# Performance work log

Hardware: AMD Instinct MI355X
Metric: run time of the kernel (lower is better)

## Reference

```python
import jax, jax.numpy as jnp
import numpy as np

D_MODEL, N_HEAD, D_HEAD = 1024, 16, 64
QLEN, MLEN, BSZ = 1024, 512, 4
KLEN = QLEN + MLEN
RLEN = QLEN + KLEN
SCALE = 1.0 / (D_HEAD ** 0.5)
LN_EPS = 1e-12


def rel_shift(x, klen):
    # x: [i, j, b, n] -> shifted [i, klen, b, n]
    i, j, b, n = x.shape
    x = x.reshape(j, i, b, n)[1:].reshape(i, j - 1, b, n)
    return x[:, :klen]


def layer_norm(x, gamma, beta, eps=LN_EPS):
    mu = jnp.mean(x, axis=-1, keepdims=True)
    var = jnp.mean(jnp.square(x - mu), axis=-1, keepdims=True)
    return (x - mu) * jax.lax.rsqrt(var + eps) * gamma + beta


def setup_inputs() -> dict:
    key = jax.random.key(0)
    ks = jax.random.split(key, 16)
    std = 0.02
    h = jax.random.normal(ks[0], (QLEN, BSZ, D_MODEL), jnp.float32)
    r = jax.random.normal(ks[1], (RLEN, BSZ, D_MODEL), jnp.float32)
    mems = jax.random.normal(ks[2], (MLEN, BSZ, D_MODEL), jnp.float32)
    # binary float mask (1 = masked), broadcast over head dim
    attn_mask = (jax.random.uniform(ks[3], (QLEN, KLEN, BSZ, 1)) < 0.1).astype(jnp.float32)
    # one-hot segment matrix over 2 segment classes
    seg_ids = jax.random.randint(ks[4], (QLEN, KLEN, BSZ), 0, 2)
    seg_mat = jax.nn.one_hot(seg_ids, 2, dtype=jnp.float32)
    Wq = std * jax.random.normal(ks[5], (D_MODEL, N_HEAD, D_HEAD), jnp.float32)
    Wk = std * jax.random.normal(ks[6], (D_MODEL, N_HEAD, D_HEAD), jnp.float32)
    Wv = std * jax.random.normal(ks[7], (D_MODEL, N_HEAD, D_HEAD), jnp.float32)
    Wo = std * jax.random.normal(ks[8], (D_MODEL, N_HEAD, D_HEAD), jnp.float32)
    Wr = std * jax.random.normal(ks[9], (D_MODEL, N_HEAD, D_HEAD), jnp.float32)
    r_w_bias = jnp.zeros((N_HEAD, D_HEAD), jnp.float32)
    r_r_bias = jnp.zeros((N_HEAD, D_HEAD), jnp.float32)
    r_s_bias = jnp.zeros((N_HEAD, D_HEAD), jnp.float32)
    seg_embed = std * jax.random.normal(ks[10], (2, N_HEAD, D_HEAD), jnp.float32)
    ln_gamma = jnp.ones((D_MODEL,), jnp.float32)
    ln_beta = jnp.zeros((D_MODEL,), jnp.float32)
    return dict(h=h, r=r, mems=mems, attn_mask=attn_mask, seg_mat=seg_mat,
                Wq=Wq, Wk=Wk, Wv=Wv, Wo=Wo, Wr=Wr,
                r_w_bias=r_w_bias, r_r_bias=r_r_bias, r_s_bias=r_s_bias,
                seg_embed=seg_embed, ln_gamma=ln_gamma, ln_beta=ln_beta)


def reference(h, r, mems, attn_mask, seg_mat, Wq, Wk, Wv, Wo, Wr,
              r_w_bias, r_r_bias, r_s_bias, seg_embed, ln_gamma, ln_beta):
    cat = jnp.concatenate([mems, h], axis=0)  # [klen, b, d_model]
    q_head = jnp.einsum('ibh,hnd->ibnd', h, Wq)
    k_head_h = jnp.einsum('jbh,hnd->jbnd', cat, Wk)
    v_head_h = jnp.einsum('jbh,hnd->jbnd', cat, Wv)
    k_head_r = jnp.einsum('jbh,hnd->jbnd', r, Wr)

    klen = k_head_h.shape[0]
    ac = jnp.einsum('ibnd,jbnd->ijbn', q_head + r_w_bias, k_head_h)
    bd = jnp.einsum('ibnd,jbnd->ijbn', q_head + r_r_bias, k_head_r)
    bd = rel_shift(bd, klen)
    ef = jnp.einsum('ibnd,snd->ibns', q_head + r_s_bias, seg_embed)
    ef = jnp.einsum('ijbs,ibns->ijbn', seg_mat, ef)

    attn_score = (ac + bd + ef) * SCALE - 1e30 * attn_mask
    attn_prob = jax.nn.softmax(attn_score, axis=1)
    attn_vec = jnp.einsum('ijbn,jbnd->ibnd', attn_prob, v_head_h)

    attn_out = jnp.einsum('ibnd,hnd->ibh', attn_vec, Wo) + h  # residual
    return layer_norm(attn_out, ln_gamma, ln_beta)
```

## Files before the change

### kernel.cpp

```cpp
#include <hip/hip_runtime.h>

typedef unsigned short u16;
typedef __attribute__((ext_vector_type(8))) short bf16x8;
typedef __attribute__((ext_vector_type(4))) float f32x4;

constexpr int DM = 1024;
constexpr int NH = 16;
constexpr int DH = 64;
constexpr int QL = 1024;
constexpr int ML = 512;
constexpr int KL = 1536;
constexpr int RL = 2560;
constexpr int BS = 4;
constexpr int JT = KL / 64;
constexpr float SCALE = 0.125f;

static __device__ __forceinline__ u16 f2bf(float f) {
    unsigned u = __float_as_uint(f);
    u += 0x7fffu + ((u >> 16) & 1u);
    return (u16)(u >> 16);
}

static __device__ __forceinline__ void glds16(const u16* g, u16* l) {
    __builtin_amdgcn_global_load_lds(
        (const __attribute__((address_space(1))) unsigned int*)g,
        (__attribute__((address_space(3))) unsigned int*)l,
        16, 0, 0);
}

__global__ __launch_bounds__(256) void prep_kernel(
    const float* __restrict__ mems, const float* __restrict__ h,
    const float* __restrict__ r, const float* __restrict__ Wo,
    const float* __restrict__ mask, const float* __restrict__ segm,
    const float* __restrict__ Wq, const float* __restrict__ Wk,
    const float* __restrict__ Wv, const float* __restrict__ Wr,
    u16* __restrict__ catb, u16* __restrict__ rb, u16* __restrict__ wob,
    u16* __restrict__ WqT, u16* __restrict__ WkT,
    u16* __restrict__ WvT, u16* __restrict__ WrT,
    ulonglong2* __restrict__ pk)
{
    __shared__ float smem[64 * 65];
    const int id = blockIdx.x;
    const int t = threadIdx.x;

    if (id < 17408) {
        const long C0 = (long)ML * BS * DM;
        const long C1 = (long)KL * BS * DM;
        const long C2 = C1 + (long)RL * BS * DM;
        long g = ((long)id * 256 + t) * 4;
        const float* src; u16* dst;
        if (g < C0)      { src = mems + g;        dst = catb + g; }
        else if (g < C1) { src = h + (g - C0);    dst = catb + g; }
        else if (g < C2) { src = r + (g - C1);    dst = rb + (g - C1); }
        else             { src = Wo + (g - C2);   dst = wob + (g - C2); }
        float4 v = *(const float4*)src;
        unsigned lo = (unsigned)f2bf(v.x) | ((unsigned)f2bf(v.y) << 16);
        unsigned hi = (unsigned)f2bf(v.z) | ((unsigned)f2bf(v.w) << 16);
        *(uint2*)dst = make_uint2(lo, hi);
        return;
    }
    if (id < 18432) {
        float (*tile)[65] = (float(*)[65])smem;
        const int local = id - 17408;
        const float* W; u16* WT;
        switch (local >> 8) {
            case 0:  W = Wq; WT = WqT; break;
            case 1:  W = Wk; WT = WkT; break;
            case 2:  W = Wv; WT = WvT; break;
            default: W = Wr; WT = WrT; break;
        }
        const int k0 = (local & 15) * 64, n0 = ((local >> 4) & 15) * 64;
        const int tr = t >> 6, tc = t & 63;
        #pragma unroll
        for (int rr = 0; rr < 16; rr++) {
            int rw = tr + rr * 4;
            tile[rw][tc] = W[(size_t)(k0 + rw) * DM + n0 + tc];
        }
        __syncthreads();
        #pragma unroll
        for (int rr = 0; rr < 16; rr++) {
            int n = tr + rr * 4;
            WT[(size_t)(n0 + n) * DM + k0 + tc] = f2bf(tile[tc][n]);
        }
        return;
    }
    {
        float* mk = smem;
        float* sg = smem + 256;
        const int local = id - 18432;
        const int i = local / JT, jt = local - i * JT;
        const size_t base = ((size_t)i * KL + jt * 64) * BS;
        mk[t] = mask[base + t];
        float2 s2 = ((const float2*)(segm + base * 2))[t];
        sg[t] = s2.y;
        __syncthreads();
        const int b = t >> 6, lane = t & 63;
        const unsigned long long mb = __ballot(mk[lane * 4 + b] > 0.5f);
        const unsigned long long sb = __ballot(sg[lane * 4 + b] > 0.5f);
        if (lane == 0) {
            ulonglong2 v; v.x = mb; v.y = sb;
            pk[((size_t)b * QL + i) * JT + jt] = v;
        }
    }
}

__global__ __launch_bounds__(256) void proj_kernel(
    const u16* __restrict__ hb, const u16* __restrict__ catb,
    const u16* __restrict__ rb,
    const u16* __restrict__ WqT, const u16* __restrict__ WkT,
    const u16* __restrict__ WvT, const u16* __restrict__ WrT,
    float* __restrict__ q_s, u16* __restrict__ k_s,
    u16* __restrict__ v_s, u16* __restrict__ kr_s)
{
    __shared__ u16 a_lds[128][32];
    __shared__ u16 b_lds[128][32];
    const int id = blockIdx.x;
    const u16 *A, *B; void* C; int SEQ, MODE, local;
    if (id < 256)       { A = hb;   B = WqT; C = q_s;  SEQ = QL; MODE = 1; local = id; }
    else if (id < 640)  { A = catb; B = WkT; C = k_s;  SEQ = KL; MODE = 2; local = id - 256; }
    else if (id < 1024) { A = catb; B = WvT; C = v_s;  SEQ = KL; MODE = 2; local = id - 640; }
    else                { A = rb;   B = WrT; C = kr_s; SEQ = RL; MODE = 2; local = id - 1024; }
    const int bm = local >> 3, bnn = local & 7;

    const int t = threadIdx.x;
    const int w = t >> 6, lane = t & 63, l15 = lane & 15, q4 = lane >> 4;
    const int wm = (w >> 1) * 64, wn = (w & 1) * 64;
    const int srow = w * 32 + (lane >> 2);
    const int scol = (lane & 3) * 8;
    const u16* Ab = A + (size_t)(bm * 128 + srow) * DM + scol;
    const u16* Bb = B + (size_t)(bnn * 128 + srow) * DM + scol;
    u16* a_dst = &a_lds[w * 32][0];
    u16* b_dst = &b_lds[w * 32][0];

    f32x4 acc[4][4] = {};

    for (int k0 = 0; k0 < DM; k0 += 32) {
        __syncthreads();
        glds16(Ab + k0,           a_dst);
        glds16(Ab + k0 + 16 * DM, a_dst + 16 * 32);
        glds16(Bb + k0,           b_dst);
        glds16(Bb + k0 + 16 * DM, b_dst + 16 * 32);
        __syncthreads();
        bf16x8 af[4], bf[4];
        #pragma unroll
        for (int rt = 0; rt < 4; rt++)
            af[rt] = *(const bf16x8*)&a_lds[wm + rt * 16 + l15][q4 * 8];
        #pragma unroll
        for (int ct = 0; ct < 4; ct++)
            bf[ct] = *(const bf16x8*)&b_lds[wn + ct * 16 + l15][q4 * 8];
        #pragma unroll
        for (int rt = 0; rt < 4; rt++)
            #pragma unroll
            for (int ct = 0; ct < 4; ct++)
                acc[rt][ct] = __builtin_amdgcn_mfma_f32_16x16x32_bf16(
                    af[rt], bf[ct], acc[rt][ct], 0, 0, 0);
    }

    #pragma unroll
    for (int rt = 0; rt < 4; rt++)
      #pragma unroll
      for (int ct = 0; ct < 4; ct++)
        #pragma unroll
        for (int rg = 0; rg < 4; rg++) {
            const int R = bm * 128 + wm + rt * 16 + q4 * 4 + rg;
            const int Cc = bnn * 128 + wn + ct * 16 + l15;
            const float v = acc[rt][ct][rg];
            const int sq = R >> 2, bb = R & 3, hn = Cc >> 6, dd = Cc & 63;
            const size_t idx = ((size_t)(bb * NH + hn) * SEQ + sq) * DH + dd;
            if (MODE == 1) ((float*)C)[idx] = v;
            else           ((u16*)C)[idx]  = f2bf(v);
        }
}

__global__ __launch_bounds__(256) void vtrans_kernel(
    const u16* __restrict__ v_s, u16* __restrict__ vt_s)
{
    __shared__ u16 tl[64][72];
    const int j0 = blockIdx.x * 64;
    const int bn = blockIdx.y;
    const u16* vin = v_s + (size_t)bn * KL * DH;
    u16* vout = vt_s + (size_t)bn * DH * KL;
    const int t = threadIdx.x;
    const int r = t >> 3, c8 = (t & 7) * 8;
    #pragma unroll
    for (int it = 0; it < 64; it += 32)
        *(uint4*)&tl[r + it][c8] = *(const uint4*)(vin + (size_t)(j0 + r + it) * DH + c8);
    __syncthreads();
    #pragma unroll
    for (int it = 0; it < 64; it += 32) {
        const int d = r + it;
        u16 tmp[8];
        #pragma unroll
        for (int jj = 0; jj < 8; jj++) tmp[jj] = tl[c8 + jj][d];
        *(uint4*)&vout[(size_t)d * KL + j0 + c8] = *(const uint4*)tmp;
    }
}

__global__ __launch_bounds__(256) void ogemm_kernel(
    const u16* __restrict__ A, const u16* __restrict__ B,
    float* __restrict__ Cout)
{
    __shared__ u16 a_lds[128][32];
    __shared__ u16 b_lds[128][32];
    const int bm = blockIdx.x, bnn = blockIdx.y;
    const int t = threadIdx.x;
    const int w = t >> 6, lane = t & 63, l15 = lane & 15, q4 = lane >> 4;
    const int wm = (w >> 1) * 64, wn = (w & 1) * 64;
    const int srow = w * 32 + (lane >> 2);
    const int scol = (lane & 3) * 8;
    const u16* Ab = A + (size_t)(bm * 128 + srow) * DM + scol;
    const u16* Bb = B + (size_t)(bnn * 128 + srow) * DM + scol;
    u16* a_dst = &a_lds[w * 32][0];
    u16* b_dst = &b_lds[w * 32][0];

    f32x4 acc[4][4] = {};

    for (int k0 = 0; k0 < DM; k0 += 32) {
        __syncthreads();
        glds16(Ab + k0,           a_dst);
        glds16(Ab + k0 + 16 * DM, a_dst + 16 * 32);
        glds16(Bb + k0,           b_dst);
        glds16(Bb + k0 + 16 * DM, b_dst + 16 * 32);
        __syncthreads();
        bf16x8 af[4], bf[4];
        #pragma unroll
        for (int rt = 0; rt < 4; rt++)
            af[rt] = *(const bf16x8*)&a_lds[wm + rt * 16 + l15][q4 * 8];
        #pragma unroll
        for (int ct = 0; ct < 4; ct++)
            bf[ct] = *(const bf16x8*)&b_lds[wn + ct * 16 + l15][q4 * 8];
        #pragma unroll
        for (int rt = 0; rt < 4; rt++)
            #pragma unroll
            for (int ct = 0; ct < 4; ct++)
                acc[rt][ct] = __builtin_amdgcn_mfma_f32_16x16x32_bf16(
                    af[rt], bf[ct], acc[rt][ct], 0, 0, 0);
    }

    #pragma unroll
    for (int rt = 0; rt < 4; rt++)
      #pragma unroll
      for (int ct = 0; ct < 4; ct++)
        #pragma unroll
        for (int rg = 0; rg < 4; rg++) {
            const int R = bm * 128 + wm + rt * 16 + q4 * 4 + rg;
            const int C = bnn * 128 + wn + ct * 16 + l15;
            Cout[(size_t)R * DM + C] = acc[rt][ct][rg];
        }
}

__global__ __launch_bounds__(256, 3) void attn_kernel(
    const float* __restrict__ q_s, const u16* __restrict__ k_s,
    const u16* __restrict__ vt_s, const u16* __restrict__ kr_s,
    const ulonglong2* __restrict__ pk,
    const float* __restrict__ rwb, const float* __restrict__ rrb,
    const float* __restrict__ rsb, const float* __restrict__ seg_embed,
    u16* __restrict__ av_s)
{
    __shared__ u16 k2[2][64][32];
    __shared__ u16 vt2[2][64][32];
    __shared__ u16 krl[128][64];
    __shared__ u16 p_lds[4][16][72];
    __shared__ float e_lds[2][64];

    const int bn = blockIdx.x;
    const int itile = blockIdx.y;
    const int b = bn >> 4, n = bn & 15;
    const int t = threadIdx.x;
    const int w = t >> 6, lane = t & 63, l15 = lane & 15, q4 = lane >> 4;
    const int i0 = itile * 64;
    const int ib = i0 + w * 16;

    const float* q_bn = q_s + (size_t)bn * QL * DH;
    const u16* k_bn   = k_s  + (size_t)bn * KL * DH;
    const u16* vt_bn  = vt_s + (size_t)bn * DH * KL;
    const u16* kr_bn  = kr_s + (size_t)bn * RL * DH;
    const ulonglong2* pk_b = pk + (size_t)b * QL * JT;

    if (t < 128) {
        const int rr = t >> 1, s = t & 1;
        const float* qrow = q_bn + (size_t)(i0 + rr) * DH;
        const float* se = seg_embed + (s * NH + n) * DH;
        const float* bias = rsb + n * DH;
        float acc = 0.f;
        #pragma unroll 16
        for (int d = 0; d < DH; d++) acc += (qrow[d] + bias[d]) * se[d];
        e_lds[s][rr] = acc;
    }

    bf16x8 qw[2], qr[2];
    {
        const float* qrow = q_bn + (size_t)(ib + l15) * DH;
        const float* bw = rwb + n * DH;
        const float* br = rrb + n * DH;
        #pragma unroll
        for (int kk = 0; kk < 2; kk++) {
            const int dbase = kk * 32 + q4 * 8;
            #pragma unroll
            for (int j = 0; j < 8; j++) {
                float qv = qrow[dbase + j];
                qw[kk][j] = (short)f2bf(qv + bw[dbase + j]);
                qr[kk][j] = (short)f2bf(qv + br[dbase + j]);
            }
        }
    }

    const int srow = lane >> 2;
    const int sseg = (lane & 3) * 8;
    const u16* kg = k_bn  + (size_t)(w * 16 + srow) * DH + sseg;
    const u16* vg = vt_bn + (size_t)(w * 16 + srow) * KL + sseg;
    u16* kd0 = &k2[0][w * 16][0];
    u16* kd1 = &k2[1][w * 16][0];
    u16* vd0 = &vt2[0][w * 16][0];
    u16* vd1 = &vt2[1][w * 16][0];

    const int krow = lane >> 3;
    const int ksrcseg = (lane & 7) ^ krow;
    u16* krd = &krl[w * 32][0];

    f32x4 o[4] = {};
    float l_r[4] = {0.f, 0.f, 0.f, 0.f};

    const int lrb = 48 - w * 16 + l15;
    const int sA = ((q4)     ^ (l15 & 7)) * 8;
    const int sB = ((q4 + 4) ^ (l15 & 7)) * 8;

    for (int jt = 0; jt < JT; jt++) {
        const int j0 = jt * 64;
        const int Pbase = j0 + QL - i0 - 63;
        __syncthreads();
        glds16(kg + (size_t)j0 * DH,      kd0);
        glds16(kg + (size_t)j0 * DH + 32, kd1);
        glds16(vg + j0,                   vd0);
        glds16(vg + j0 + 32,              vd1);
        {
            const u16* krg = kr_bn + (size_t)(Pbase + w * 32 + krow) * DH + ksrcseg * 8;
            #pragma unroll
            for (int m = 0; m < 4; m++)
                glds16(krg + (size_t)m * 8 * DH, krd + m * 8 * 64);
        }
        ulonglong2 mp[4];
        #pragma unroll
        for (int rg = 0; rg < 4; rg++)
            mp[rg] = pk_b[(size_t)(ib + q4 * 4 + rg) * JT + jt];
        __syncthreads();

        f32x4 sac[4] = {};
        #pragma unroll
        for (int ct = 0; ct < 4; ct++) {
            bf16x8 kb0 = *(const bf16x8*)&k2[0][ct * 16 + l15][q4 * 8];
            bf16x8 kb1 = *(const bf16x8*)&k2[1][ct * 16 + l15][q4 * 8];
            sac[ct] = __builtin_amdgcn_mfma_f32_16x16x32_bf16(qw[0], kb0, sac[ct], 0, 0, 0);
            sac[ct] = __builtin_amdgcn_mfma_f32_16x16x32_bf16(qw[1], kb1, sac[ct], 0, 0, 0);
        }

        f32x4 bacc[5] = {};
        #pragma unroll
        for (int wc = 0; wc < 5; wc++) {
            bf16x8 b0 = *(const bf16x8*)&krl[lrb + wc * 16][sA];
            bf16x8 b1 = *(const bf16x8*)&krl[lrb + wc * 16][sB];
            bacc[wc] = __builtin_amdgcn_mfma_f32_16x16x32_bf16(qr[0], b0, bacc[wc], 0, 0, 0);
            bacc[wc] = __builtin_amdgcn_mfma_f32_16x16x32_bf16(qr[1], b1, bacc[wc], 0, 0, 0);
        }

        #pragma unroll
        for (int rg = 0; rg < 4; rg++) {
            const int row = q4 * 4 + rg;
            const int v = l15 + 15 - row;
            const int srcl = (q4 << 4) | (v & 15);
            float sh[5];
            #pragma unroll
            for (int w5 = 0; w5 < 5; w5++)
                sh[w5] = __shfl(bacc[w5][rg], srcl, 64);
            const float e0 = e_lds[0][w * 16 + row];
            const float e1 = e_lds[1][w * 16 + row];
            float s0 = 0.f;
            #pragma unroll
            for (int ct = 0; ct < 4; ct++) {
                const float bd = (v < 16) ? sh[ct] : sh[ct + 1];
                const int bit = ct * 16 + l15;
                const float ef = ((mp[rg].y >> bit) & 1ull) ? e1 : e0;
                const float s = (sac[ct][rg] + bd + ef) * SCALE;
                float p = __expf(s);
                p = ((mp[rg].x >> bit) & 1ull) ? 0.f : p;
                p_lds[w][row][ct * 16 + l15] = f2bf(p);
                s0 += p;
            }
            l_r[rg] += s0;
        }

        #pragma unroll
        for (int kk = 0; kk < 2; kk++) {
            bf16x8 pf = *(const bf16x8*)&p_lds[w][l15][kk * 32 + q4 * 8];
            #pragma unroll
            for (int dt = 0; dt < 4; dt++) {
                bf16x8 vf = *(const bf16x8*)&vt2[kk][dt * 16 + l15][q4 * 8];
                o[dt] = __builtin_amdgcn_mfma_f32_16x16x32_bf16(pf, vf, o[dt], 0, 0, 0);
            }
        }
    }

    #pragma unroll
    for (int rg = 0; rg < 4; rg++) {
        #pragma unroll
        for (int off = 1; off < 16; off <<= 1)
            l_r[rg] += __shfl_xor(l_r[rg], off, 64);
        l_r[rg] = 1.f / l_r[rg];
    }
    #pragma unroll
    for (int dt = 0; dt < 4; dt++)
        #pragma unroll
        for (int rg = 0; rg < 4; rg++) {
            const int row = q4 * 4 + rg;
            const int ii = ib + row;
            const int d = dt * 16 + l15;
            const float v = o[dt][rg] * l_r[rg];
            av_s[(size_t)(ii * BS + b) * DM + n * DH + d] = f2bf(v);
        }
}

__global__ __launch_bounds__(256) void ln_kernel(
    const float* __restrict__ ao, const float* __restrict__ h,
    const float* __restrict__ gamma, const float* __restrict__ beta,
    float* __restrict__ out)
{
    __shared__ float red[8];
    const int row = blockIdx.x, t = threadIdx.x;
    const float* a  = ao + (size_t)row * DM;
    const float* hh = h  + (size_t)row * DM;
    float4 av = *(const float4*)(a + t * 4);
    float4 hv = *(const float4*)(hh + t * 4);
    const float x0 = av.x + hv.x, x1 = av.y + hv.y;
    const float x2 = av.z + hv.z, x3 = av.w + hv.w;
    float s = x0 + x1 + x2 + x3;
    float s2 = x0 * x0 + x1 * x1 + x2 * x2 + x3 * x3;
    #pragma unroll
    for (int off = 1; off < 64; off <<= 1) {
        s  += __shfl_xor(s, off, 64);
        s2 += __shfl_xor(s2, off, 64);
    }
    const int w = t >> 6;
    if ((t & 63) == 0) { red[w] = s; red[4 + w] = s2; }
    __syncthreads();
    s  = red[0] + red[1] + red[2] + red[3];
    s2 = red[4] + red[5] + red[6] + red[7];
    const float mu = s * (1.f / DM);
    const float var = s2 * (1.f / DM) - mu * mu;
    const float rstd = rsqrtf(var + 1e-12f);
    float4 g  = *(const float4*)(gamma + t * 4);
    float4 bb = *(const float4*)(beta + t * 4);
    float4 ov;
    ov.x = (x0 - mu) * rstd * g.x + bb.x;
    ov.y = (x1 - mu) * rstd * g.y + bb.y;
    ov.z = (x2 - mu) * rstd * g.z + bb.z;
    ov.w = (x3 - mu) * rstd * g.w + bb.w;
    *(float4*)(out + (size_t)row * DM + t * 4) = ov;
}

extern "C" void kernel_launch(void* const* d_in, const int* in_sizes, int n_in,
                              void* d_out, int out_size, void* d_ws, size_t ws_size,
                              hipStream_t stream) {
    (void)in_sizes; (void)n_in; (void)out_size; (void)ws_size;
    const float* h    = (const float*)d_in[0];
    const float* r    = (const float*)d_in[1];
    const float* mems = (const float*)d_in[2];
    const float* mask = (const float*)d_in[3];
    const float* segm = (const float*)d_in[4];
    const float* Wq   = (const float*)d_in[5];
    const float* Wk   = (const float*)d_in[6];
    const float* Wv   = (const float*)d_in[7];
    const float* Wo   = (const float*)d_in[8];
    const float* Wr   = (const float*)d_in[9];
    const float* rwb  = (const float*)d_in[10];
    const float* rrb  = (const float*)d_in[11];
    const float* rsb  = (const float*)d_in[12];
    const float* semb = (const float*)d_in[13];
    const float* gam  = (const float*)d_in[14];
    const float* bet  = (const float*)d_in[15];
    float* out = (float*)d_out;

    char* wsb = (char*)d_ws;
    size_t off = 0;
    auto alloc = [&](size_t bytes) -> void* {
        void* p = wsb + off; off += (bytes + 255) & ~(size_t)255; return p;
    };
    u16* catb = (u16*)alloc((size_t)KL * BS * DM * 2);
    u16* rb   = (u16*)alloc((size_t)RL * BS * DM * 2);
    u16* WqT  = (u16*)alloc((size_t)DM * DM * 2);
    u16* WkT  = (u16*)alloc((size_t)DM * DM * 2);
    u16* WvT  = (u16*)alloc((size_t)DM * DM * 2);
    u16* WrT  = (u16*)alloc((size_t)DM * DM * 2);
    u16* WoB  = (u16*)alloc((size_t)DM * DM * 2);
    float* q_s = (float*)alloc((size_t)BS * NH * QL * DH * 4);
    u16* k_s  = (u16*)alloc((size_t)BS * NH * KL * DH * 2);
    u16* vt_s = (u16*)alloc((size_t)BS * NH * KL * DH * 2);
    u16* kr_s = (u16*)alloc((size_t)BS * NH * RL * DH * 2 + 8192);
    u16* av_s = (u16*)alloc((size_t)QL * BS * DM * 2);
    float* ao_s = (float*)alloc((size_t)QL * BS * DM * 4);
    ulonglong2* pk = (ulonglong2*)alloc((size_t)BS * QL * JT * 16);
    u16* v_s = (u16*)ao_s;

    prep_kernel<<<43008, 256, 0, stream>>>(mems, h, r, Wo, mask, segm,
                                           Wq, Wk, Wv, Wr,
                                           catb, rb, WoB,
                                           WqT, WkT, WvT, WrT, pk);
    const u16* hb = catb + (size_t)2048 * DM;
    proj_kernel<<<1664, 256, 0, stream>>>(hb, catb, rb, WqT, WkT, WvT, WrT,
                                          q_s, k_s, v_s, kr_s);
    vtrans_kernel<<<dim3(JT, 64), 256, 0, stream>>>(v_s, vt_s);
    attn_kernel<<<dim3(64, 16), 256, 0, stream>>>(q_s, k_s, vt_s, kr_s, pk,
                                                  rwb, rrb, rsb, semb, av_s);
    ogemm_kernel<<<dim3(32, 8), 256, 0, stream>>>(av_s, WoB, ao_s);
    ln_kernel<<<4096, 256, 0, stream>>>(ao_s, h, gam, bet, out);
}
```

Baseline: 530.0 us.

## Enlarge attention query tile to 128 rows with 8 warps sharing K/V loads

```diff
diff --git a/kernel.cpp b/kernel.cpp
--- a/kernel.cpp
+++ b/kernel.cpp
@@ -249,7 +249,7 @@
         }
 }
 
-__global__ __launch_bounds__(256, 3) void attn_kernel(
+__global__ __launch_bounds__(512, 4) void attn_kernel(
     const float* __restrict__ q_s, const u16* __restrict__ k_s,
     const u16* __restrict__ vt_s, const u16* __restrict__ kr_s,
     const ulonglong2* __restrict__ pk,
@@ -259,16 +259,15 @@
 {
     __shared__ u16 k2[2][64][32];
     __shared__ u16 vt2[2][64][32];
-    __shared__ u16 krl[128][64];
-    __shared__ u16 p_lds[4][16][72];
-    __shared__ float e_lds[2][64];
+    __shared__ u16 krl[256][64];
+    __shared__ u16 p_lds[8][16][72];
+    __shared__ float e_lds[2][128];
 
     const int bn = blockIdx.x;
-    const int itile = blockIdx.y;
     const int b = bn >> 4, n = bn & 15;
     const int t = threadIdx.x;
     const int w = t >> 6, lane = t & 63, l15 = lane & 15, q4 = lane >> 4;
-    const int i0 = itile * 64;
+    const int i0 = blockIdx.y * 128;
     const int ib = i0 + w * 16;
 
     const float* q_bn = q_s + (size_t)bn * QL * DH;
@@ -277,7 +276,7 @@
     const u16* kr_bn  = kr_s + (size_t)bn * RL * DH;
     const ulonglong2* pk_b = pk + (size_t)b * QL * JT;
 
-    if (t < 128) {
+    if (t < 256) {
         const int rr = t >> 1, s = t & 1;
         const float* qrow = q_bn + (size_t)(i0 + rr) * DH;
         const float* se = seg_embed + (s * NH + n) * DH;
@@ -307,37 +306,39 @@
 
     const int srow = lane >> 2;
     const int sseg = (lane & 3) * 8;
-    const u16* kg = k_bn  + (size_t)(w * 16 + srow) * DH + sseg;
-    const u16* vg = vt_bn + (size_t)(w * 16 + srow) * KL + sseg;
-    u16* kd0 = &k2[0][w * 16][0];
-    u16* kd1 = &k2[1][w * 16][0];
-    u16* vd0 = &vt2[0][w * 16][0];
-    u16* vd1 = &vt2[1][w * 16][0];
-
     const int krow = lane >> 3;
     const int ksrcseg = (lane & 7) ^ krow;
-    u16* krd = &krl[w * 32][0];
 
     f32x4 o[4] = {};
     float l_r[4] = {0.f, 0.f, 0.f, 0.f};
 
-    const int lrb = 48 - w * 16 + l15;
+    const int lrb = 144 - w * 16 + l15;
     const int sA = ((q4)     ^ (l15 & 7)) * 8;
     const int sB = ((q4 + 4) ^ (l15 & 7)) * 8;
 
     for (int jt = 0; jt < JT; jt++) {
         const int j0 = jt * 64;
-        const int Pbase = j0 + QL - i0 - 63;
-        __syncthreads();
-        glds16(kg + (size_t)j0 * DH,      kd0);
-        glds16(kg + (size_t)j0 * DH + 32, kd1);
-        glds16(vg + j0,                   vd0);
-        glds16(vg + j0 + 32,              vd1);
-        {
-            const u16* krg = kr_bn + (size_t)(Pbase + w * 32 + krow) * DH + ksrcseg * 8;
-            #pragma unroll
-            for (int m = 0; m < 4; m++)
-                glds16(krg + (size_t)m * 8 * DH, krd + m * 8 * 64);
+        const int Pbase = j0 + QL - i0 - 159;
+        __syncthreads();
+        if (w < 4) {
+            #pragma unroll
+            for (int g = 0; g < 4; g++) {
+                const int rr = g * 16 + srow;
+                if (w == 0)
+                    glds16(k_bn + (size_t)(j0 + rr) * DH + sseg,       &k2[0][g * 16][0]);
+                else if (w == 1)
+                    glds16(k_bn + (size_t)(j0 + rr) * DH + 32 + sseg,  &k2[1][g * 16][0]);
+                else if (w == 2)
+                    glds16(vt_bn + (size_t)rr * KL + j0 + sseg,        &vt2[0][g * 16][0]);
+                else
+                    glds16(vt_bn + (size_t)rr * KL + j0 + 32 + sseg,   &vt2[1][g * 16][0]);
+            }
+        } else {
+            const int rbase = (w - 4) * 64;
+            const u16* krg = kr_bn + ((size_t)(Pbase + rbase + krow)) * DH + ksrcseg * 8;
+            #pragma unroll
+            for (int g = 0; g < 8; g++)
+                glds16(krg + (size_t)g * 8 * DH, &krl[rbase + g * 8][0]);
         }
         ulonglong2 mp[4];
         #pragma unroll
@@ -494,7 +495,8 @@
     float* q_s = (float*)alloc((size_t)BS * NH * QL * DH * 4);
     u16* k_s  = (u16*)alloc((size_t)BS * NH * KL * DH * 2);
     u16* vt_s = (u16*)alloc((size_t)BS * NH * KL * DH * 2);
-    u16* kr_s = (u16*)alloc((size_t)BS * NH * RL * DH * 2 + 8192);
+    (void)alloc(32768);
+    u16* kr_s = (u16*)alloc((size_t)BS * NH * RL * DH * 2 + 16384);
     u16* av_s = (u16*)alloc((size_t)QL * BS * DM * 2);
     float* ao_s = (float*)alloc((size_t)QL * BS * DM * 4);
     ulonglong2* pk = (ulonglong2*)alloc((size_t)BS * QL * JT * 16);
@@ -508,8 +510,8 @@
     proj_kernel<<<1664, 256, 0, stream>>>(hb, catb, rb, WqT, WkT, WvT, WrT,
                                           q_s, k_s, v_s, kr_s);
     vtrans_kernel<<<dim3(JT, 64), 256, 0, stream>>>(v_s, vt_s);
-    attn_kernel<<<dim3(64, 16), 256, 0, stream>>>(q_s, k_s, vt_s, kr_s, pk,
-                                                  rwb, rrb, rsb, semb, av_s);
+    attn_kernel<<<dim3(64, 8), 512, 0, stream>>>(q_s, k_s, vt_s, kr_s, pk,
+                                                 rwb, rrb, rsb, semb, av_s);
     ogemm_kernel<<<dim3(32, 8), 256, 0, stream>>>(av_s, WoB, ao_s);
     ln_kernel<<<4096, 256, 0, stream>>>(ao_s, h, gam, bet, out);
 }
```

New measurement: 610.4 us. 1.15x slower.
